# Kernel tuning notes

Measured on AMD Instinct MI355X. Metric: run time of the kernel, lower is better.

## Reference

```python
import jax, jax.numpy as jnp
import numpy as np

NDIR = 6      # build_tree.num_directions()
IDIM = 256
ODIM = 512
B, L, NCH = 8, 4096, 8192


def setup_inputs() -> dict:
    key = jax.random.key(0)
    ks = jax.random.split(key, 9)
    last = jax.random.normal(ks[0], (B, NCH, IDIM), dtype=jnp.float32)
    child_l = jax.random.randint(ks[1], (L,), 0, NCH, dtype=jnp.int32)
    child_r = jax.random.randint(ks[2], (L,), 0, NCH, dtype=jnp.int32)
    vec = jax.random.randint(ks[3], (B, L), 0, NCH, dtype=jnp.int32)
    drev = jax.random.randint(ks[4], (NCH,), 0, 2, dtype=jnp.int32)
    dmap = jax.random.randint(ks[5], (NCH,), 0, NDIR, dtype=jnp.int32)
    # merge FC params: ndir independent Linear(2*idim -> odim) + PReLU(init=relu_weight)
    scale = 1.0 / np.sqrt(2 * IDIM)
    W_merge = jax.random.uniform(ks[6], (NDIR, ODIM, 2 * IDIM), jnp.float32, -scale, scale)
    b_merge = jax.random.uniform(ks[7], (NDIR, ODIM), jnp.float32, -scale, scale)
    alpha_merge = jnp.full((NDIR,), 0.005, dtype=jnp.float32)  # PReLU weight (relu_weight)
    return {"last": last, "W_merge": W_merge, "b_merge": b_merge,
            "alpha_merge": alpha_merge, "child_l": child_l, "child_r": child_r,
            "vec": vec, "drev": drev, "dmap": dmap}


def reference(last, W_merge, b_merge, alpha_merge, child_l, child_r, vec, drev, dmap):
    # child gathers: [B, L, idim]
    lch = last[:, child_l]
    rch = last[:, child_r]
    # per-element direction-reverse blending
    d = drev[vec][:, :, None].astype(last.dtype)          # [B, L, 1]
    a = lch * (1.0 - d) + rch * d
    b = rch * (1.0 - d) + lch * d
    ans = jnp.concatenate([a, b], axis=-1)                # [B, L, 2*idim]
    # routed merge: compute all ndir linears, then select per element (ndir is small)
    y_all = jnp.einsum('bli,doi->bldo', ans, W_merge) + b_merge   # [B, L, ndir, odim]
    dir_idx = dmap[vec]                                   # [B, L] in [0, ndir)
    y = jnp.take_along_axis(y_all, dir_idx[:, :, None, None], axis=2)[:, :, 0]  # [B, L, odim]
    alpha = alpha_merge[dir_idx][:, :, None]              # per-element PReLU slope
    return jnp.where(y > 0, y, alpha * y)
```

## Files before the change

kernel.cpp:

```cpp
#include <hip/hip_runtime.h>
#include <hip/hip_bf16.h>

#define BB 8
#define LL 4096
#define NCH 8192
#define IDIM 256
#define KDIM 512
#define ODIM 512
#define NDIR 6
#define TOT (BB * LL)

#define CAP 8192
#define IDX_OFF 64
#define ROWS_OFF (64 + 8 * CAP)
#define WS_LAST_OFF (64 + 16 * CAP)
#define LAST_ELEMS (BB * NCH * IDIM)
#define W_ELEMS (NDIR * ODIM * KDIM)
#define N_LAST8 (LAST_ELEMS / 8)
#define N_W8 (W_ELEMS / 8)

#define MTILES (TOT / 64 + NDIR)
typedef short short8 __attribute__((ext_vector_type(8)));
typedef float floatx4 __attribute__((ext_vector_type(4)));

__device__ inline void async_copy16(const void* g, void* l) {
  __builtin_amdgcn_global_load_lds(
      (const __attribute__((address_space(1))) void*)g,
      (__attribute__((address_space(3))) void*)l, 16, 0, 0);
}

__device__ inline void cvt8(const float* __restrict__ src,
                            __hip_bfloat16* __restrict__ dst, int i) {
  const floatx4* s = (const floatx4*)src;
  floatx4 a = s[2 * i];
  floatx4 b = s[2 * i + 1];
  union { short8 v; __hip_bfloat16 h[8]; } u;
  u.h[0] = __float2bfloat16(a[0]); u.h[1] = __float2bfloat16(a[1]);
  u.h[2] = __float2bfloat16(a[2]); u.h[3] = __float2bfloat16(a[3]);
  u.h[4] = __float2bfloat16(b[0]); u.h[5] = __float2bfloat16(b[1]);
  u.h[6] = __float2bfloat16(b[2]); u.h[7] = __float2bfloat16(b[3]);
  ((short8*)dst)[i] = u.v;
}

__global__ __launch_bounds__(256) void prep_kernel(
    const float* __restrict__ last, const float* __restrict__ W,
    const int* __restrict__ vec, const int* __restrict__ child_l,
    const int* __restrict__ child_r, const int* __restrict__ drev,
    const int* __restrict__ dmap, int* __restrict__ ws) {
  __hip_bfloat16* last_bf = (__hip_bfloat16*)(ws + WS_LAST_OFF);
  __hip_bfloat16* W_bf = last_bf + LAST_ELEMS;
  int gid = blockIdx.x * 256 + threadIdx.x;
  if (gid < N_LAST8) {
    cvt8(last, last_bf, gid);
  } else if (gid < N_LAST8 + N_W8) {
    cvt8(W, W_bf, gid - N_LAST8);
  } else {
    __shared__ int lcnt[8];
    __shared__ int gbase[8];
    int tid = threadIdx.x;
    if (tid < 8) lcnt[tid] = 0;
    __syncthreads();
    int lin = gid - (N_LAST8 + N_W8);
    int l = lin & (LL - 1);
    int v = vec[lin];
    int dir = dmap[v] & 7;
    int sw = drev[v];
    int cl = child_l[l];
    int cr = child_r[l];
    int r0 = sw ? cr : cl;
    int r1 = sw ? cl : cr;
    int pos = atomicAdd(&lcnt[dir], 1);
    __syncthreads();
    if (tid < 8) gbase[tid] = lcnt[tid] ? atomicAdd(&ws[tid], lcnt[tid]) : 0;
    __syncthreads();
    int slot = dir * CAP + gbase[dir] + pos;
    ws[IDX_OFF + slot] = lin;
    ws[ROWS_OFF + slot] = r0 | (r1 << 16);
  }
}

__global__ __launch_bounds__(64) void gemm_kernel(
    const float* __restrict__ bias, const float* __restrict__ alpha_m,
    const int* __restrict__ ws, float* __restrict__ out) {
  __shared__ __hip_bfloat16 Als[2][64 * 64];

  int flat = blockIdx.y * 8 + blockIdx.x;
  int swz = (flat & 7) * MTILES + (flat >> 3);
  const int mt = swz >> 3;
  const int nt = swz & 7;

  int d = -1, count = 0, m_base = 0;
  {
    int tb = 0;
    for (int dd = 0; dd < 8; ++dd) {
      int c = ws[dd];
      int ntile = (c + 63) >> 6;
      if (mt < tb + ntile) { d = dd; count = c; m_base = (mt - tb) * 64; break; }
      tb += ntile;
    }
  }
  if (d < 0) return;

  const int* idxA = ws + IDX_OFF + d * CAP;
  const int* rowsA = ws + ROWS_OFF + d * CAP;
  const char* last_bf = (const char*)(ws + WS_LAST_OFF);
  const char* W_bf = last_bf + (long long)LAST_ELEMS * 2;

  const int lane = threadIdx.x;
  const int lane15 = lane & 15;
  const int quad = lane >> 4;

  int aoff0[8], aoff1[8];
  const int xu2 = (((lane & 7) ^ (lane >> 3)) * 8) * 2;
#pragma unroll
  for (int i = 0; i < 8; ++i) {
    int gr = m_base + i * 8 + (lane >> 3);
    if (gr >= count) gr = count - 1;
    int lin = idxA[gr] & (TOT - 1);
    int rr = rowsA[gr];
    int b = lin >> 12;
    aoff0[i] = (b * NCH + (rr & (NCH - 1))) * (IDIM * 2) + xu2;
    aoff1[i] = (b * NCH + ((rr >> 16) & (NCH - 1))) * (IDIM * 2) + xu2;
  }
  int boff[4];
#pragma unroll
  for (int j = 0; j < 4; ++j)
    boff[j] = ((d * ODIM + nt * 64 + j * 16 + lane15) * KDIM + quad * 8) * 2;

  floatx4 acc[4][4] = {};
  const int lx = lane15 & 7;

#pragma unroll
  for (int i = 0; i < 8; ++i)
    async_copy16(last_bf + aoff0[i], &Als[0][i * 512]);

#pragma unroll
  for (int t = 0; t < 8; ++t) {
    const int cur = t & 1;
    short8 bfr[2][4];
#pragma unroll
    for (int s = 0; s < 2; ++s)
#pragma unroll
      for (int j = 0; j < 4; ++j)
        bfr[s][j] = *(const short8*)(W_bf + boff[j] + (t * 64 + s * 32) * 2);

    asm volatile("s_waitcnt lgkmcnt(0)" ::: "memory");
    if (t < 7) {
      const int tn = t + 1;
      const int ko = (tn & 3) * (64 * 2);
#pragma unroll
      for (int i = 0; i < 8; ++i)
        async_copy16(last_bf + (tn < 4 ? aoff0[i] : aoff1[i]) + ko,
                     &Als[cur ^ 1][i * 512]);
      asm volatile("s_waitcnt vmcnt(8)" ::: "memory");
    } else {
      asm volatile("s_waitcnt vmcnt(0)" ::: "memory");
    }
    __builtin_amdgcn_sched_barrier(0);

#pragma unroll
    for (int s = 0; s < 2; ++s) {
      const int xcol = ((quad + 4 * s) ^ lx) * 8;
      short8 a[4];
#pragma unroll
      for (int i = 0; i < 4; ++i)
        a[i] = *(const short8*)&Als[cur][(i * 16 + lane15) * 64 + xcol];
#pragma unroll
      for (int i = 0; i < 4; ++i)
#pragma unroll
        for (int j = 0; j < 4; ++j)
          acc[i][j] = __builtin_amdgcn_mfma_f32_16x16x32_bf16(a[i], bfr[s][j], acc[i][j], 0, 0, 0);
    }
  }

  const float alpha = alpha_m[d];
  float bj[4];
#pragma unroll
  for (int j = 0; j < 4; ++j)
    bj[j] = bias[d * ODIM + nt * 64 + j * 16 + lane15];

#pragma unroll
  for (int i = 0; i < 4; ++i) {
#pragma unroll
    for (int reg = 0; reg < 4; ++reg) {
      int row_id = m_base + i * 16 + quad * 4 + reg;
      if (row_id >= count) continue;
      int lin = idxA[row_id] & (TOT - 1);
      float* orow = out + (long long)lin * ODIM + nt * 64;
#pragma unroll
      for (int j = 0; j < 4; ++j) {
        float y = acc[i][j][reg] + bj[j];
        y = y > 0.f ? y : alpha * y;
        orow[j * 16 + lane15] = y;
      }
    }
  }
}

extern "C" void kernel_launch(void* const* d_in, const int* in_sizes, int n_in,
                              void* d_out, int out_size, void* d_ws, size_t ws_size,
                              hipStream_t stream) {
  const float* last = (const float*)d_in[0];
  const float* W = (const float*)d_in[1];
  const float* bias = (const float*)d_in[2];
  const float* alpha = (const float*)d_in[3];
  const int* child_l = (const int*)d_in[4];
  const int* child_r = (const int*)d_in[5];
  const int* vec = (const int*)d_in[6];
  const int* drev = (const int*)d_in[7];
  const int* dmap = (const int*)d_in[8];

  int* ws = (int*)d_ws;

  hipMemsetAsync(ws, 0, 64 * sizeof(int), stream);
  int prep_blocks = N_LAST8 / 256 + N_W8 / 256 + TOT / 256;
  prep_kernel<<<prep_blocks, 256, 0, stream>>>(last, W, vec, child_l, child_r,
                                               drev, dmap, ws);
  dim3 grid(8, MTILES, 1);
  gemm_kernel<<<grid, 64, 0, stream>>>(bias, alpha, ws, (float*)d_out);
}
```

Baseline: 182.8 us.

## Gather fp32 activations directly in GEMM and use 128x512 tiles per block

Drops the bulk fp32-to-bf16 conversion pass over the whole activation tensor in the prep kernel. The GEMM now gathers the fp32 child rows straight into LDS and converts them to bf16 while loading MFMA fragments. Each 512-thread block covers a 128-row tile across all 512 output columns, so every gathered A row is read once instead of once per column tile. In exchange the A bytes per gathered row double, LDS use grows to 64KB, block barriers are added, and grid parallelism falls to about 262 blocks.

Measured after the change: 211.0 us. 1.15x slower.

```diff
diff --git a/kernel.cpp b/kernel.cpp
--- a/kernel.cpp
+++ b/kernel.cpp
@@ -13,13 +13,12 @@
 #define CAP 8192
 #define IDX_OFF 64
 #define ROWS_OFF (64 + 8 * CAP)
-#define WS_LAST_OFF (64 + 16 * CAP)
-#define LAST_ELEMS (BB * NCH * IDIM)
+#define WS_W_OFF (64 + 16 * CAP)
 #define W_ELEMS (NDIR * ODIM * KDIM)
-#define N_LAST8 (LAST_ELEMS / 8)
 #define N_W8 (W_ELEMS / 8)
 
-#define MTILES (TOT / 64 + NDIR)
+#define MTILES (TOT / 128 + NDIR)
+
 typedef short short8 __attribute__((ext_vector_type(8)));
 typedef float floatx4 __attribute__((ext_vector_type(4)));
 
@@ -43,24 +42,21 @@
 }
 
 __global__ __launch_bounds__(256) void prep_kernel(
-    const float* __restrict__ last, const float* __restrict__ W,
-    const int* __restrict__ vec, const int* __restrict__ child_l,
-    const int* __restrict__ child_r, const int* __restrict__ drev,
-    const int* __restrict__ dmap, int* __restrict__ ws) {
-  __hip_bfloat16* last_bf = (__hip_bfloat16*)(ws + WS_LAST_OFF);
-  __hip_bfloat16* W_bf = last_bf + LAST_ELEMS;
+    const float* __restrict__ W, const int* __restrict__ vec,
+    const int* __restrict__ child_l, const int* __restrict__ child_r,
+    const int* __restrict__ drev, const int* __restrict__ dmap,
+    int* __restrict__ ws) {
+  __hip_bfloat16* W_bf = (__hip_bfloat16*)(ws + WS_W_OFF);
   int gid = blockIdx.x * 256 + threadIdx.x;
-  if (gid < N_LAST8) {
-    cvt8(last, last_bf, gid);
-  } else if (gid < N_LAST8 + N_W8) {
-    cvt8(W, W_bf, gid - N_LAST8);
+  if (gid < N_W8) {
+    cvt8(W, W_bf, gid);
   } else {
     __shared__ int lcnt[8];
     __shared__ int gbase[8];
     int tid = threadIdx.x;
     if (tid < 8) lcnt[tid] = 0;
     __syncthreads();
-    int lin = gid - (N_LAST8 + N_W8);
+    int lin = gid - N_W8;
     int l = lin & (LL - 1);
     int v = vec[lin];
     int dir = dmap[v] & 7;
@@ -79,23 +75,20 @@
   }
 }
 
-__global__ __launch_bounds__(64) void gemm_kernel(
-    const float* __restrict__ bias, const float* __restrict__ alpha_m,
-    const int* __restrict__ ws, float* __restrict__ out) {
-  __shared__ __hip_bfloat16 Als[2][64 * 64];
-
-  int flat = blockIdx.y * 8 + blockIdx.x;
-  int swz = (flat & 7) * MTILES + (flat >> 3);
-  const int mt = swz >> 3;
-  const int nt = swz & 7;
-
+__global__ __launch_bounds__(512) void gemm_kernel(
+    const float* __restrict__ last, const float* __restrict__ bias,
+    const float* __restrict__ alpha_m, const int* __restrict__ ws,
+    float* __restrict__ out) {
+  __shared__ float Als[2][128 * 64];
+
+  const int mt = blockIdx.x;
   int d = -1, count = 0, m_base = 0;
   {
     int tb = 0;
     for (int dd = 0; dd < 8; ++dd) {
       int c = ws[dd];
-      int ntile = (c + 63) >> 6;
-      if (mt < tb + ntile) { d = dd; count = c; m_base = (mt - tb) * 64; break; }
+      int ntile = (c + 127) >> 7;
+      if (mt < tb + ntile) { d = dd; count = c; m_base = (mt - tb) * 128; break; }
       tb += ntile;
     }
   }
@@ -103,92 +96,103 @@
 
   const int* idxA = ws + IDX_OFF + d * CAP;
   const int* rowsA = ws + ROWS_OFF + d * CAP;
-  const char* last_bf = (const char*)(ws + WS_LAST_OFF);
-  const char* W_bf = last_bf + (long long)LAST_ELEMS * 2;
-
-  const int lane = threadIdx.x;
+  const char* W_bf = (const char*)(ws + WS_W_OFF);
+  const char* lastc = (const char*)last;
+
+  const int tid = threadIdx.x;
+  const int wave = __builtin_amdgcn_readfirstlane(tid >> 6);
+  const int lane = tid & 63;
   const int lane15 = lane & 15;
   const int quad = lane >> 4;
-
-  int aoff0[8], aoff1[8];
-  const int xu2 = (((lane & 7) ^ (lane >> 3)) * 8) * 2;
-#pragma unroll
-  for (int i = 0; i < 8; ++i) {
-    int gr = m_base + i * 8 + (lane >> 3);
+  const int wm = wave >> 2;
+  const int wn = wave & 3;
+
+  int asrc0[4], asrc1[4];
+  int ldsoff[4];
+#pragma unroll
+  for (int g = 0; g < 4; ++g) {
+    int r = wave * 16 + g * 4 + (lane >> 4);
+    ldsoff[g] = (wave * 16 + g * 4) * 64;
+    int gr = m_base + r;
     if (gr >= count) gr = count - 1;
     int lin = idxA[gr] & (TOT - 1);
     int rr = rowsA[gr];
     int b = lin >> 12;
-    aoff0[i] = (b * NCH + (rr & (NCH - 1))) * (IDIM * 2) + xu2;
-    aoff1[i] = (b * NCH + ((rr >> 16) & (NCH - 1))) * (IDIM * 2) + xu2;
-  }
-  int boff[4];
-#pragma unroll
-  for (int j = 0; j < 4; ++j)
-    boff[j] = ((d * ODIM + nt * 64 + j * 16 + lane15) * KDIM + quad * 8) * 2;
-
-  floatx4 acc[4][4] = {};
-  const int lx = lane15 & 7;
-
-#pragma unroll
-  for (int i = 0; i < 8; ++i)
-    async_copy16(last_bf + aoff0[i], &Als[0][i * 512]);
+    int off = (((lane & 15) ^ (r & 15)) * 16);
+    asrc0[g] = (b * NCH + (rr & (NCH - 1))) * 1024 + off;
+    asrc1[g] = (b * NCH + ((rr >> 16) & (NCH - 1))) * 1024 + off;
+  }
+  int boff[8];
+#pragma unroll
+  for (int j = 0; j < 8; ++j)
+    boff[j] = ((d * ODIM + wn * 128 + j * 16 + lane15) * KDIM + quad * 8) * 2;
+
+  floatx4 acc[4][8] = {};
+
+#pragma unroll
+  for (int g = 0; g < 4; ++g)
+    async_copy16(lastc + asrc0[g], &Als[0][ldsoff[g]]);
 
 #pragma unroll
   for (int t = 0; t < 8; ++t) {
     const int cur = t & 1;
-    short8 bfr[2][4];
+    short8 bfr[2][8];
 #pragma unroll
     for (int s = 0; s < 2; ++s)
 #pragma unroll
-      for (int j = 0; j < 4; ++j)
+      for (int j = 0; j < 8; ++j)
         bfr[s][j] = *(const short8*)(W_bf + boff[j] + (t * 64 + s * 32) * 2);
-
-    asm volatile("s_waitcnt lgkmcnt(0)" ::: "memory");
     if (t < 7) {
       const int tn = t + 1;
-      const int ko = (tn & 3) * (64 * 2);
-#pragma unroll
-      for (int i = 0; i < 8; ++i)
-        async_copy16(last_bf + (tn < 4 ? aoff0[i] : aoff1[i]) + ko,
-                     &Als[cur ^ 1][i * 512]);
-      asm volatile("s_waitcnt vmcnt(8)" ::: "memory");
+      const int ko = (tn & 3) * 256;
+#pragma unroll
+      for (int g = 0; g < 4; ++g)
+        async_copy16(lastc + (tn < 4 ? asrc0[g] : asrc1[g]) + ko,
+                     &Als[cur ^ 1][ldsoff[g]]);
+      asm volatile("s_waitcnt vmcnt(4)" ::: "memory");
     } else {
       asm volatile("s_waitcnt vmcnt(0)" ::: "memory");
     }
     __builtin_amdgcn_sched_barrier(0);
+    __builtin_amdgcn_s_barrier();
 
 #pragma unroll
     for (int s = 0; s < 2; ++s) {
-      const int xcol = ((quad + 4 * s) ^ lx) * 8;
-      short8 a[4];
-#pragma unroll
-      for (int i = 0; i < 4; ++i)
-        a[i] = *(const short8*)&Als[cur][(i * 16 + lane15) * 64 + xcol];
-#pragma unroll
-      for (int i = 0; i < 4; ++i)
-#pragma unroll
-        for (int j = 0; j < 4; ++j)
-          acc[i][j] = __builtin_amdgcn_mfma_f32_16x16x32_bf16(a[i], bfr[s][j], acc[i][j], 0, 0, 0);
-    }
+#pragma unroll
+      for (int i = 0; i < 4; ++i) {
+        const int r = wm * 64 + i * 16 + lane15;
+        const int ulo = (2 * (quad + 4 * s)) ^ lane15;
+        const floatx4 lo = *(const floatx4*)&Als[cur][r * 64 + ulo * 4];
+        const floatx4 hi = *(const floatx4*)&Als[cur][r * 64 + (ulo ^ 1) * 4];
+        union { short8 v; __hip_bfloat16 h[8]; } u;
+        u.h[0] = __float2bfloat16(lo[0]); u.h[1] = __float2bfloat16(lo[1]);
+        u.h[2] = __float2bfloat16(lo[2]); u.h[3] = __float2bfloat16(lo[3]);
+        u.h[4] = __float2bfloat16(hi[0]); u.h[5] = __float2bfloat16(hi[1]);
+        u.h[6] = __float2bfloat16(hi[2]); u.h[7] = __float2bfloat16(hi[3]);
+#pragma unroll
+        for (int j = 0; j < 8; ++j)
+          acc[i][j] = __builtin_amdgcn_mfma_f32_16x16x32_bf16(u.v, bfr[s][j], acc[i][j], 0, 0, 0);
+      }
+    }
+    __builtin_amdgcn_s_barrier();
   }
 
   const float alpha = alpha_m[d];
-  float bj[4];
-#pragma unroll
-  for (int j = 0; j < 4; ++j)
-    bj[j] = bias[d * ODIM + nt * 64 + j * 16 + lane15];
+  float bj[8];
+#pragma unroll
+  for (int j = 0; j < 8; ++j)
+    bj[j] = bias[d * ODIM + wn * 128 + j * 16 + lane15];
 
 #pragma unroll
   for (int i = 0; i < 4; ++i) {
 #pragma unroll
     for (int reg = 0; reg < 4; ++reg) {
-      int row_id = m_base + i * 16 + quad * 4 + reg;
+      int row_id = m_base + wm * 64 + i * 16 + quad * 4 + reg;
       if (row_id >= count) continue;
       int lin = idxA[row_id] & (TOT - 1);
-      float* orow = out + (long long)lin * ODIM + nt * 64;
-#pragma unroll
-      for (int j = 0; j < 4; ++j) {
+      float* orow = out + (long long)lin * ODIM + wn * 128;
+#pragma unroll
+      for (int j = 0; j < 8; ++j) {
         float y = acc[i][j][reg] + bj[j];
         y = y > 0.f ? y : alpha * y;
         orow[j * 16 + lane15] = y;
@@ -213,9 +217,7 @@
   int* ws = (int*)d_ws;
 
   hipMemsetAsync(ws, 0, 64 * sizeof(int), stream);
-  int prep_blocks = N_LAST8 / 256 + N_W8 / 256 + TOT / 256;
-  prep_kernel<<<prep_blocks, 256, 0, stream>>>(last, W, vec, child_l, child_r,
-                                               drev, dmap, ws);
-  dim3 grid(8, MTILES, 1);
-  gemm_kernel<<<grid, 64, 0, stream>>>(bias, alpha, ws, (float*)d_out);
-}
+  prep_kernel<<<(N_W8 / 256) + (TOT / 256), 256, 0, stream>>>(
+      W, vec, child_l, child_r, drev, dmap, ws);
+  gemm_kernel<<<MTILES, 512, 0, stream>>>(last, bias, alpha, ws, (float*)d_out);
+}
```
